# Kernel tuning notes

Measured on AMD Instinct MI355X. Metric: run time of the kernel, lower is better.

Reference implementation:

```python
import jax, jax.numpy as jnp
import numpy as np

B, N, IN_F, OUT_F, HEADS = 16, 256, 128, 64, 4
NEG = -9e15

def setup_inputs() -> dict:
    key = jax.random.key(0)
    ks = jax.random.split(key, 7)
    x = jax.random.normal(ks[0], (B, N, IN_F), dtype=jnp.float32)
    adj = jax.random.randint(ks[1], (B, N, N), 0, 2, dtype=jnp.int32)
    adj_in = jax.random.randint(ks[2], (B, N, N), 0, 2, dtype=jnp.int32)
    adj_out = jax.random.randint(ks[3], (B, N, N), 0, 2, dtype=jnp.int32)
    # params: W linear (no bias), a linear (with bias)
    gain = 1.414
    lim_W = gain * np.sqrt(6.0 / (IN_F + OUT_F))
    W = jax.random.uniform(ks[4], (OUT_F, IN_F), jnp.float32, -lim_W, lim_W)
    lim_A = gain * np.sqrt(6.0 / (2 * OUT_F + 3 * HEADS))
    A = jax.random.uniform(ks[5], (3 * HEADS, 2 * OUT_F), jnp.float32, -lim_A, lim_A)
    a_b = jax.random.uniform(ks[6], (3 * HEADS,), jnp.float32, -1.0, 1.0) / np.sqrt(2 * OUT_F)
    return {"x": x, "adj": adj, "adj_in": adj_in, "adj_out": adj_out,
            "W": W, "A": A, "a_b": a_b}

def reference(x, adj, adj_in, adj_out, W, A, a_b):
    # h = W(input): [B, N, OUT_F]
    h = jnp.einsum('bni,oi->bno', x, W)
    # additive attention: a(cat[h_i, h_j]) = h_i @ A1^T + h_j @ A2^T + b
    A1, A2 = A[:, :OUT_F], A[:, OUT_F:]
    e_src = jnp.einsum('bnd,hd->bnh', h, A1)  # depends on row i
    e_dst = jnp.einsum('bnd,hd->bnh', h, A2)  # depends on col j
    e = e_src[:, :, None, :] + e_dst[:, None, :, :] + a_b  # [B, N, N, 3H]
    e = jax.nn.leaky_relu(e, negative_slope=0.01)
    e = jnp.transpose(e, (0, 3, 1, 2))  # [B, 3H, N, N]
    # tripled masks: [adj]*H ++ [adj_in]*H ++ [adj_out]*H along head axis
    mask = jnp.concatenate([
        jnp.repeat(adj[:, None], HEADS, axis=1),
        jnp.repeat(adj_in[:, None], HEADS, axis=1),
        jnp.repeat(adj_out[:, None], HEADS, axis=1)], axis=1)  # [B, 3H, N, N]
    att = jnp.where(mask > 0, e, jnp.float32(NEG))
    att = jax.nn.softmax(att, axis=-1)
    # dropout omitted (eval mode)
    h_prime = jnp.einsum('bhij,bjd->bhid', att, h).mean(axis=1)  # [B, N, OUT_F]
    return h_prime
```

## Files before the change

### kernel.cpp

```cpp
#include <hip/hip_runtime.h>

#define L2E 1.44269504088896340736f

typedef __attribute__((ext_vector_type(8))) short bf16x8;
typedef __attribute__((ext_vector_type(4))) float f32x4;

__device__ __forceinline__ unsigned bf16_rne(float v) {
    unsigned x = __float_as_uint(v);
    return (x + 0x7FFFu + ((x >> 16) & 1u)) >> 16;
}

__device__ __forceinline__ void cvt_hilo4(float4 v, uint2* hi, uint2* lo) {
    unsigned h0 = bf16_rne(v.x), h1 = bf16_rne(v.y), h2 = bf16_rne(v.z), h3 = bf16_rne(v.w);
    float f0 = __uint_as_float(h0 << 16), f1 = __uint_as_float(h1 << 16);
    float f2 = __uint_as_float(h2 << 16), f3 = __uint_as_float(h3 << 16);
    unsigned l0 = bf16_rne(v.x - f0), l1 = bf16_rne(v.y - f1);
    unsigned l2 = bf16_rne(v.z - f2), l3 = bf16_rne(v.w - f3);
    hi->x = h0 | (h1 << 16); hi->y = h2 | (h3 << 16);
    lo->x = l0 | (l1 << 16); lo->y = l2 | (l3 << 16);
}

__global__ __launch_bounds__(256) void k1_proj(
    const float* __restrict__ x, const float* __restrict__ W, const float* __restrict__ A,
    unsigned short* __restrict__ hTg, float* __restrict__ esrc, float* __restrict__ edstT)
{
    __shared__ unsigned short xh[16 * 136], xl[16 * 136];
    __shared__ unsigned short wh[64 * 136], wl[64 * 136];
    __shared__ unsigned short Ach[32 * 72], Acl[32 * 72];
    __shared__ unsigned short hsh[16 * 72], hsl[16 * 72];

    const int t = threadIdx.x;
    const int row0 = blockIdx.x * 16;
    const int b = row0 >> 8;
    const int ibase = row0 & 255;

#pragma unroll
    for (int p = 0; p < 2; ++p) {
        int q = t + 256 * p;
        int r = q >> 5, c = (q & 31) * 4;
        float4 v = *(const float4*)&x[row0 * 128 + 4 * q];
        uint2 hi, lo; cvt_hilo4(v, &hi, &lo);
        *(uint2*)&xh[r * 136 + c] = hi;
        *(uint2*)&xl[r * 136 + c] = lo;
    }
#pragma unroll
    for (int p = 0; p < 8; ++p) {
        int q = t + 256 * p;
        int r = q >> 5, c = (q & 31) * 4;
        float4 v = *(const float4*)&W[4 * q];
        uint2 hi, lo; cvt_hilo4(v, &hi, &lo);
        *(uint2*)&wh[r * 136 + c] = hi;
        *(uint2*)&wl[r * 136 + c] = lo;
    }
#pragma unroll
    for (int p = 0; p < 2; ++p) {
        int q = t + 256 * p;
        int n = q >> 4, d = (q & 15) * 4;
        float4 v = make_float4(0.f, 0.f, 0.f, 0.f);
        if (n < 24) {
            int nn = (n < 12) ? n : n - 12;
            v = *(const float4*)&A[nn * 128 + ((n < 12) ? 0 : 64) + d];
        }
        uint2 hi, lo; cvt_hilo4(v, &hi, &lo);
        *(uint2*)&Ach[n * 72 + d] = hi;
        *(uint2*)&Acl[n * 72 + d] = lo;
    }
    __syncthreads();

    const int lane = t & 63;
    const int wv = t >> 6;
    const int ml = lane & 15, kb = lane >> 4;

    f32x4 acc = {0.f, 0.f, 0.f, 0.f};
#pragma unroll
    for (int ks = 0; ks < 4; ++ks) {
        const int ko = ks * 32 + kb * 8;
        bf16x8 axh = *(const bf16x8*)&xh[ml * 136 + ko];
        bf16x8 axl = *(const bf16x8*)&xl[ml * 136 + ko];
        bf16x8 bwh = *(const bf16x8*)&wh[(wv * 16 + ml) * 136 + ko];
        bf16x8 bwl = *(const bf16x8*)&wl[(wv * 16 + ml) * 136 + ko];
        acc = __builtin_amdgcn_mfma_f32_16x16x32_bf16(axh, bwh, acc, 0, 0, 0);
        acc = __builtin_amdgcn_mfma_f32_16x16x32_bf16(axh, bwl, acc, 0, 0, 0);
        acc = __builtin_amdgcn_mfma_f32_16x16x32_bf16(axl, bwh, acc, 0, 0, 0);
    }
#pragma unroll
    for (int r = 0; r < 4; ++r) {
        const int m = kb * 4 + r, c = wv * 16 + ml;
        unsigned hi = bf16_rne(acc[r]);
        float hif = __uint_as_float(hi << 16);
        hsh[m * 72 + c] = (unsigned short)hi;
        hsl[m * 72 + c] = (unsigned short)bf16_rne(acc[r] - hif);
    }
    __syncthreads();

    if (wv < 2) {
        f32x4 e4 = {0.f, 0.f, 0.f, 0.f};
#pragma unroll
        for (int ks = 0; ks < 2; ++ks) {
            const int ko = ks * 32 + kb * 8;
            bf16x8 ah = *(const bf16x8*)&hsh[ml * 72 + ko];
            bf16x8 al = *(const bf16x8*)&hsl[ml * 72 + ko];
            bf16x8 bh = *(const bf16x8*)&Ach[(wv * 16 + ml) * 72 + ko];
            bf16x8 bl = *(const bf16x8*)&Acl[(wv * 16 + ml) * 72 + ko];
            e4 = __builtin_amdgcn_mfma_f32_16x16x32_bf16(ah, bh, e4, 0, 0, 0);
            e4 = __builtin_amdgcn_mfma_f32_16x16x32_bf16(ah, bl, e4, 0, 0, 0);
            e4 = __builtin_amdgcn_mfma_f32_16x16x32_bf16(al, bh, e4, 0, 0, 0);
        }
#pragma unroll
        for (int r = 0; r < 4; ++r) {
            const int m = kb * 4 + r, n = wv * 16 + ml;
            if (n < 12)
                esrc[(row0 + m) * 12 + n] = e4[r];
            else if (n < 24)
                edstT[(b * 12 + (n - 12)) * 256 + ibase + m] = e4[r];
        }
    }

#pragma unroll
    for (int it = 0; it < 4; ++it) {
        int e2 = t + 256 * it;
        int d = e2 >> 4, jj = e2 & 15;
        hTg[(b * 64 + d) * 256 + ibase + jj] = hsh[jj * 72 + d];
    }
}

__global__ __launch_bounds__(256) void k2_attn(
    const int* __restrict__ adj, const int* __restrict__ adjin, const int* __restrict__ adjout,
    const float* __restrict__ esrc, const float* __restrict__ edstT,
    const unsigned short* __restrict__ hTg, const float* __restrict__ ab,
    float* __restrict__ out)
{
    __shared__ unsigned short Ph[16 * 264];
    __shared__ unsigned short Pl_[16 * 264];

    const int t = threadIdx.x;
    const int b  = blockIdx.x >> 6;
    const int i0 = (blockIdx.x & 63) * 4;
    const int lane = t & 63;
    const int wv = t >> 6;
    const int gi = b * 256 + i0 + wv;

    const int4 M0 = *(const int4*)(adj    + (size_t)gi * 256 + 4 * lane);
    const int4 M1 = *(const int4*)(adjin  + (size_t)gi * 256 + 4 * lane);
    const int4 M2 = *(const int4*)(adjout + (size_t)gi * 256 + 4 * lane);
    const float mA[4] = {(float)M0.x, (float)M0.y, (float)M0.z, (float)M0.w};
    const float mB[4] = {(float)M1.x, (float)M1.y, (float)M1.z, (float)M1.w};
    const float mC[4] = {(float)M2.x, (float)M2.y, (float)M2.z, (float)M2.w};

    const float* es = esrc + (size_t)gi * 12;
    float e0[12];
#pragma unroll
    for (int hh = 0; hh < 12; ++hh) e0[hh] = es[hh] + ab[hh];

    float Pacc[4] = {0.f, 0.f, 0.f, 0.f};
#pragma unroll
    for (int hh = 0; hh < 12; ++hh) {
        const float4 ev = *(const float4*)&edstT[(size_t)(b * 12 + hh) * 256 + 4 * lane];
        float v0 = e0[hh] + ev.x, v1 = e0[hh] + ev.y, v2 = e0[hh] + ev.z, v3 = e0[hh] + ev.w;
        v0 = v0 > 0.f ? v0 : 0.01f * v0;
        v1 = v1 > 0.f ? v1 : 0.01f * v1;
        v2 = v2 > 0.f ? v2 : 0.01f * v2;
        v3 = v3 > 0.f ? v3 : 0.01f * v3;
        const float m0 = (hh < 4) ? mA[0] : (hh < 8) ? mB[0] : mC[0];
        const float m1 = (hh < 4) ? mA[1] : (hh < 8) ? mB[1] : mC[1];
        const float m2 = (hh < 4) ? mA[2] : (hh < 8) ? mB[2] : mC[2];
        const float m3 = (hh < 4) ? mA[3] : (hh < 8) ? mB[3] : mC[3];
        float p0 = __builtin_amdgcn_exp2f(v0 * L2E) * m0;
        float p1 = __builtin_amdgcn_exp2f(v1 * L2E) * m1;
        float p2 = __builtin_amdgcn_exp2f(v2 * L2E) * m2;
        float p3 = __builtin_amdgcn_exp2f(v3 * L2E) * m3;
        float s = (p0 + p1) + (p2 + p3);
#pragma unroll
        for (int off = 32; off >= 1; off >>= 1)
            s += __shfl_xor(s, off);
        const float rinv = __builtin_amdgcn_rcpf(s);
        Pacc[0] += p0 * rinv;
        Pacc[1] += p1 * rinv;
        Pacc[2] += p2 * rinv;
        Pacc[3] += p3 * rinv;
    }
    {
        unsigned h0 = bf16_rne(Pacc[0]), h1 = bf16_rne(Pacc[1]);
        unsigned h2 = bf16_rne(Pacc[2]), h3 = bf16_rne(Pacc[3]);
        unsigned l0 = bf16_rne(Pacc[0] - __uint_as_float(h0 << 16));
        unsigned l1 = bf16_rne(Pacc[1] - __uint_as_float(h1 << 16));
        unsigned l2 = bf16_rne(Pacc[2] - __uint_as_float(h2 << 16));
        unsigned l3 = bf16_rne(Pacc[3] - __uint_as_float(h3 << 16));
        uint2 hw; hw.x = h0 | (h1 << 16); hw.y = h2 | (h3 << 16);
        uint2 lw; lw.x = l0 | (l1 << 16); lw.y = l2 | (l3 << 16);
        *(uint2*)&Ph[wv * 264 + 4 * lane]  = hw;
        *(uint2*)&Pl_[wv * 264 + 4 * lane] = lw;
    }
    __syncthreads();

    const int ml = lane & 15, kb = lane >> 4;
    const unsigned short* hTb = hTg + ((size_t)b * 64 + wv * 16 + ml) * 256;
    f32x4 acc = {0.f, 0.f, 0.f, 0.f};
#pragma unroll
    for (int ks = 0; ks < 8; ++ks) {
        const int ko = ks * 32 + kb * 8;
        bf16x8 bh = *(const bf16x8*)&hTb[ko];
        bf16x8 ah = *(const bf16x8*)&Ph[ml * 264 + ko];
        bf16x8 al = *(const bf16x8*)&Pl_[ml * 264 + ko];
        acc = __builtin_amdgcn_mfma_f32_16x16x32_bf16(ah, bh, acc, 0, 0, 0);
        acc = __builtin_amdgcn_mfma_f32_16x16x32_bf16(al, bh, acc, 0, 0, 0);
    }
    if (kb == 0) {
#pragma unroll
        for (int r = 0; r < 4; ++r)
            out[(size_t)(b * 256 + i0 + r) * 64 + wv * 16 + ml] = acc[r] * (1.0f / 12.0f);
    }
}

extern "C" void kernel_launch(void* const* d_in, const int* in_sizes, int n_in,
                              void* d_out, int out_size, void* d_ws, size_t ws_size,
                              hipStream_t stream) {
    const float* x    = (const float*)d_in[0];
    const int*   adj  = (const int*)d_in[1];
    const int*   adji = (const int*)d_in[2];
    const int*   adjo = (const int*)d_in[3];
    const float* W    = (const float*)d_in[4];
    const float* A    = (const float*)d_in[5];
    const float* ab   = (const float*)d_in[6];
    float* out = (float*)d_out;

    unsigned short* hTg = (unsigned short*)d_ws;
    float* esrc  = (float*)((char*)d_ws + (512 << 10));
    float* edstT = (float*)((char*)d_ws + (704 << 10));

    k1_proj<<<256, 256, 0, stream>>>(x, W, A, hTg, esrc, edstT);
    k2_attn<<<1024, 256, 0, stream>>>(adj, adji, adjo, esrc, edstT, hTg, ab, out);
}
```

Before: 19.73 us.

## Process eight rows per attention block, drop low-bf16 split, prefold bias and log2e

The attention kernel now handles 8 query rows per block, two per wave with 32 lanes each, so it launches half as many blocks and each lane does 8 columns. This makes better use of the 16-row MFMA tile, which was previously only a quarter filled. The hi/lo bf16 split of the probability matrix is dropped, halving both the MFMA work and the LDS traffic, at the cost of some precision. The bias add and the log2(e) scaling move into the projection kernel's epilogue, and the hT transpose store is widened to 32-bit writes.

New measurement: 18.00 us. 8.8% less time.

```diff
diff --git a/kernel.cpp b/kernel.cpp
--- a/kernel.cpp
+++ b/kernel.cpp
@@ -22,6 +22,7 @@
 
 __global__ __launch_bounds__(256) void k1_proj(
     const float* __restrict__ x, const float* __restrict__ W, const float* __restrict__ A,
+    const float* __restrict__ ab,
     unsigned short* __restrict__ hTg, float* __restrict__ esrc, float* __restrict__ edstT)
 {
     __shared__ unsigned short xh[16 * 136], xl[16 * 136];
@@ -110,86 +111,92 @@
         for (int r = 0; r < 4; ++r) {
             const int m = kb * 4 + r, n = wv * 16 + ml;
             if (n < 12)
-                esrc[(row0 + m) * 12 + n] = e4[r];
+                esrc[(row0 + m) * 12 + n] = (e4[r] + ab[n]) * L2E;
             else if (n < 24)
-                edstT[(b * 12 + (n - 12)) * 256 + ibase + m] = e4[r];
-        }
-    }
-
-#pragma unroll
-    for (int it = 0; it < 4; ++it) {
+                edstT[(b * 12 + (n - 12)) * 256 + ibase + m] = e4[r] * L2E;
+        }
+    }
+
+#pragma unroll
+    for (int it = 0; it < 2; ++it) {
         int e2 = t + 256 * it;
-        int d = e2 >> 4, jj = e2 & 15;
-        hTg[(b * 64 + d) * 256 + ibase + jj] = hsh[jj * 72 + d];
+        int d = e2 >> 3, j2 = (e2 & 7) * 2;
+        unsigned lo16 = hsh[j2 * 72 + d], hi16 = hsh[(j2 + 1) * 72 + d];
+        *(unsigned*)&hTg[(b * 64 + d) * 256 + ibase + j2] = lo16 | (hi16 << 16);
     }
 }
 
 __global__ __launch_bounds__(256) void k2_attn(
     const int* __restrict__ adj, const int* __restrict__ adjin, const int* __restrict__ adjout,
     const float* __restrict__ esrc, const float* __restrict__ edstT,
-    const unsigned short* __restrict__ hTg, const float* __restrict__ ab,
+    const unsigned short* __restrict__ hTg,
     float* __restrict__ out)
 {
     __shared__ unsigned short Ph[16 * 264];
-    __shared__ unsigned short Pl_[16 * 264];
 
     const int t = threadIdx.x;
-    const int b  = blockIdx.x >> 6;
-    const int i0 = (blockIdx.x & 63) * 4;
+    const int b  = blockIdx.x >> 5;
+    const int i0 = (blockIdx.x & 31) * 8;
     const int lane = t & 63;
     const int wv = t >> 6;
-    const int gi = b * 256 + i0 + wv;
-
-    const int4 M0 = *(const int4*)(adj    + (size_t)gi * 256 + 4 * lane);
-    const int4 M1 = *(const int4*)(adjin  + (size_t)gi * 256 + 4 * lane);
-    const int4 M2 = *(const int4*)(adjout + (size_t)gi * 256 + 4 * lane);
-    const float mA[4] = {(float)M0.x, (float)M0.y, (float)M0.z, (float)M0.w};
-    const float mB[4] = {(float)M1.x, (float)M1.y, (float)M1.z, (float)M1.w};
-    const float mC[4] = {(float)M2.x, (float)M2.y, (float)M2.z, (float)M2.w};
-
-    const float* es = esrc + (size_t)gi * 12;
-    float e0[12];
-#pragma unroll
-    for (int hh = 0; hh < 12; ++hh) e0[hh] = es[hh] + ab[hh];
-
-    float Pacc[4] = {0.f, 0.f, 0.f, 0.f};
+    const int g = lane >> 5;
+    const int q = lane & 31;
+    const int row = wv * 2 + g;
+    const int gi = b * 256 + i0 + row;
+
+    {
+        uint4* z = (uint4*)&Ph[8 * 264];
+        if (t < 264) z[t] = make_uint4(0, 0, 0, 0);
+    }
+
+    const int4* mp0 = (const int4*)(adj    + (size_t)gi * 256 + 8 * q);
+    const int4* mp1 = (const int4*)(adjin  + (size_t)gi * 256 + 8 * q);
+    const int4* mp2 = (const int4*)(adjout + (size_t)gi * 256 + 8 * q);
+    int4 Ma0 = mp0[0], Ma1 = mp0[1];
+    int4 Mb0 = mp1[0], Mb1 = mp1[1];
+    int4 Mc0 = mp2[0], Mc1 = mp2[1];
+    float fm[3][8];
+    fm[0][0] = (float)Ma0.x; fm[0][1] = (float)Ma0.y; fm[0][2] = (float)Ma0.z; fm[0][3] = (float)Ma0.w;
+    fm[0][4] = (float)Ma1.x; fm[0][5] = (float)Ma1.y; fm[0][6] = (float)Ma1.z; fm[0][7] = (float)Ma1.w;
+    fm[1][0] = (float)Mb0.x; fm[1][1] = (float)Mb0.y; fm[1][2] = (float)Mb0.z; fm[1][3] = (float)Mb0.w;
+    fm[1][4] = (float)Mb1.x; fm[1][5] = (float)Mb1.y; fm[1][6] = (float)Mb1.z; fm[1][7] = (float)Mb1.w;
+    fm[2][0] = (float)Mc0.x; fm[2][1] = (float)Mc0.y; fm[2][2] = (float)Mc0.z; fm[2][3] = (float)Mc0.w;
+    fm[2][4] = (float)Mc1.x; fm[2][5] = (float)Mc1.y; fm[2][6] = (float)Mc1.z; fm[2][7] = (float)Mc1.w;
+
+    const float4* ep = (const float4*)(esrc + (size_t)gi * 12);
+    const float4 eA = ep[0], eB = ep[1], eC = ep[2];
+    const float e0[12] = {eA.x, eA.y, eA.z, eA.w, eB.x, eB.y, eB.z, eB.w, eC.x, eC.y, eC.z, eC.w};
+
+    float Pacc[8] = {0.f, 0.f, 0.f, 0.f, 0.f, 0.f, 0.f, 0.f};
 #pragma unroll
     for (int hh = 0; hh < 12; ++hh) {
-        const float4 ev = *(const float4*)&edstT[(size_t)(b * 12 + hh) * 256 + 4 * lane];
-        float v0 = e0[hh] + ev.x, v1 = e0[hh] + ev.y, v2 = e0[hh] + ev.z, v3 = e0[hh] + ev.w;
-        v0 = v0 > 0.f ? v0 : 0.01f * v0;
-        v1 = v1 > 0.f ? v1 : 0.01f * v1;
-        v2 = v2 > 0.f ? v2 : 0.01f * v2;
-        v3 = v3 > 0.f ? v3 : 0.01f * v3;
-        const float m0 = (hh < 4) ? mA[0] : (hh < 8) ? mB[0] : mC[0];
-        const float m1 = (hh < 4) ? mA[1] : (hh < 8) ? mB[1] : mC[1];
-        const float m2 = (hh < 4) ? mA[2] : (hh < 8) ? mB[2] : mC[2];
-        const float m3 = (hh < 4) ? mA[3] : (hh < 8) ? mB[3] : mC[3];
-        float p0 = __builtin_amdgcn_exp2f(v0 * L2E) * m0;
-        float p1 = __builtin_amdgcn_exp2f(v1 * L2E) * m1;
-        float p2 = __builtin_amdgcn_exp2f(v2 * L2E) * m2;
-        float p3 = __builtin_amdgcn_exp2f(v3 * L2E) * m3;
-        float s = (p0 + p1) + (p2 + p3);
-#pragma unroll
-        for (int off = 32; off >= 1; off >>= 1)
+        const int grp = hh >> 2;
+        const float4* evp = (const float4*)(edstT + (size_t)(b * 12 + hh) * 256 + 8 * q);
+        const float4 ev0 = evp[0], ev1 = evp[1];
+        const float evv[8] = {ev0.x, ev0.y, ev0.z, ev0.w, ev1.x, ev1.y, ev1.z, ev1.w};
+        float p[8], s = 0.f;
+#pragma unroll
+        for (int k = 0; k < 8; ++k) {
+            float v = e0[hh] + evv[k];
+            v = fmaxf(v, 0.01f * v);
+            p[k] = __builtin_amdgcn_exp2f(v) * fm[grp][k];
+            s += p[k];
+        }
+#pragma unroll
+        for (int off = 16; off >= 1; off >>= 1)
             s += __shfl_xor(s, off);
         const float rinv = __builtin_amdgcn_rcpf(s);
-        Pacc[0] += p0 * rinv;
-        Pacc[1] += p1 * rinv;
-        Pacc[2] += p2 * rinv;
-        Pacc[3] += p3 * rinv;
+#pragma unroll
+        for (int k = 0; k < 8; ++k)
+            Pacc[k] += p[k] * rinv;
     }
     {
-        unsigned h0 = bf16_rne(Pacc[0]), h1 = bf16_rne(Pacc[1]);
-        unsigned h2 = bf16_rne(Pacc[2]), h3 = bf16_rne(Pacc[3]);
-        unsigned l0 = bf16_rne(Pacc[0] - __uint_as_float(h0 << 16));
-        unsigned l1 = bf16_rne(Pacc[1] - __uint_as_float(h1 << 16));
-        unsigned l2 = bf16_rne(Pacc[2] - __uint_as_float(h2 << 16));
-        unsigned l3 = bf16_rne(Pacc[3] - __uint_as_float(h3 << 16));
-        uint2 hw; hw.x = h0 | (h1 << 16); hw.y = h2 | (h3 << 16);
-        uint2 lw; lw.x = l0 | (l1 << 16); lw.y = l2 | (l3 << 16);
-        *(uint2*)&Ph[wv * 264 + 4 * lane]  = hw;
-        *(uint2*)&Pl_[wv * 264 + 4 * lane] = lw;
+        uint4 pk;
+        pk.x = bf16_rne(Pacc[0]) | (bf16_rne(Pacc[1]) << 16);
+        pk.y = bf16_rne(Pacc[2]) | (bf16_rne(Pacc[3]) << 16);
+        pk.z = bf16_rne(Pacc[4]) | (bf16_rne(Pacc[5]) << 16);
+        pk.w = bf16_rne(Pacc[6]) | (bf16_rne(Pacc[7]) << 16);
+        *(uint4*)&Ph[row * 264 + 8 * q] = pk;
     }
     __syncthreads();
 
@@ -201,14 +208,14 @@
         const int ko = ks * 32 + kb * 8;
         bf16x8 bh = *(const bf16x8*)&hTb[ko];
         bf16x8 ah = *(const bf16x8*)&Ph[ml * 264 + ko];
-        bf16x8 al = *(const bf16x8*)&Pl_[ml * 264 + ko];
         acc = __builtin_amdgcn_mfma_f32_16x16x32_bf16(ah, bh, acc, 0, 0, 0);
-        acc = __builtin_amdgcn_mfma_f32_16x16x32_bf16(al, bh, acc, 0, 0, 0);
-    }
-    if (kb == 0) {
-#pragma unroll
-        for (int r = 0; r < 4; ++r)
-            out[(size_t)(b * 256 + i0 + r) * 64 + wv * 16 + ml] = acc[r] * (1.0f / 12.0f);
+    }
+    if (kb < 2) {
+#pragma unroll
+        for (int r = 0; r < 4; ++r) {
+            const int m = kb * 4 + r;
+            out[(size_t)(b * 256 + i0 + m) * 64 + wv * 16 + ml] = acc[r] * (1.0f / 12.0f);
+        }
     }
 }
 
@@ -228,6 +235,6 @@
     float* esrc  = (float*)((char*)d_ws + (512 << 10));
     float* edstT = (float*)((char*)d_ws + (704 << 10));
 
-    k1_proj<<<256, 256, 0, stream>>>(x, W, A, hTg, esrc, edstT);
-    k2_attn<<<1024, 256, 0, stream>>>(adj, adji, adjo, esrc, edstT, hTg, ab, out);
-}
+    k1_proj<<<256, 256, 0, stream>>>(x, W, A, ab, hTg, esrc, edstT);
+    k2_attn<<<512, 256, 0, stream>>>(adj, adji, adjo, esrc, edstT, hTg, out);
+}
```
